# Kernel optimization log

Hardware: AMD Instinct MI355X
Metric: run time of the kernel (lower is better)

The kernel has to match this reference:

```python
import jax, jax.numpy as jnp
import numpy as np
import math

N_NODES = 50000
N_EDGES = 800000
D_IN = 128
HID = 128  # layer dims: 128 -> 128 -> 64 -> 32


def _glorot(key, fan_in, fan_out):
    lim = math.sqrt(6.0 / (fan_in + fan_out))
    return jax.random.uniform(key, (fan_in, fan_out), jnp.float32, -lim, lim)


def setup_inputs() -> dict:
    key = jax.random.key(0)
    ks = jax.random.split(key, 9)
    x = jax.random.normal(ks[0], (N_NODES, D_IN), dtype=jnp.float32)
    edge_index = jax.random.randint(ks[1], (2, N_EDGES), 0, N_NODES, dtype=jnp.int64)
    edge_attr = jax.random.uniform(ks[2], (N_EDGES,), dtype=jnp.float32)
    return {
        "x": x,
        "edge_index": edge_index,
        "edge_attr": edge_attr,
        "W1": _glorot(ks[3], D_IN, HID),      "b1": jnp.zeros((HID,), jnp.float32),
        "W2": _glorot(ks[4], HID, HID // 2),  "b2": jnp.zeros((HID // 2,), jnp.float32),
        "W3": _glorot(ks[5], HID // 2, HID // 4), "b3": jnp.zeros((HID // 4,), jnp.float32),
    }


def _gcn_conv(h, W, b, src, dst, norm, n_nodes):
    # GCNConv: linear transform, then normalized scatter-add aggregation, then bias
    h = h @ W                                   # [N, F_out]
    msg = h[src] * norm[:, None]                # gather + scale, [E', F_out]
    out = jax.ops.segment_sum(msg, dst, num_segments=n_nodes)  # scatter-add
    return out + b


def reference(x, edge_index, edge_attr, W1, b1, W2, b2, W3, b3):
    n = x.shape[0]
    # add self-loops with weight 1.0 (PyG GCNConv default)
    loop = jnp.arange(n, dtype=edge_index.dtype)
    src = jnp.concatenate([edge_index[0], loop])
    dst = jnp.concatenate([edge_index[1], loop])
    w = jnp.concatenate([edge_attr, jnp.ones((n,), edge_attr.dtype)])
    # symmetric normalization: D^{-1/2} A_hat D^{-1/2}
    deg = jax.ops.segment_sum(w, dst, num_segments=n)
    dinv = jnp.where(deg > 0, jax.lax.rsqrt(jnp.maximum(deg, 1e-30)), 0.0)
    norm = dinv[src] * w * dinv[dst]            # [E + N]

    h = jax.nn.relu(_gcn_conv(x, W1, b1, src, dst, norm, n))
    # dropout is identity in eval mode
    h = jax.nn.relu(_gcn_conv(h, W2, b2, src, dst, norm, n))
    h = _gcn_conv(h, W3, b3, src, dst, norm, n)
    return h
```

## Files before the change

### kernel.cpp

```cpp
#include <hip/hip_runtime.h>
#include <hip/hip_bf16.h>

#define BLK 256
#define SCAT_NB 512
#define BIN_SHIFT 8

typedef unsigned short ushort_t;
typedef unsigned int uint_t;
typedef unsigned long long ull_t;
typedef __attribute__((ext_vector_type(8))) short bf16x8;
typedef __attribute__((ext_vector_type(4))) float f32x4;

static __device__ __forceinline__ float bf2f(ushort_t u) {
    return __uint_as_float((uint_t)u << 16);
}
static __device__ __forceinline__ ushort_t f2bf(float f) {
    __hip_bfloat16 h = __float2bfloat16(f);
    return *reinterpret_cast<ushort_t*>(&h);
}


__global__ __launch_bounds__(256) void k_pre(const int* __restrict__ eidx,
                                             int* __restrict__ bcnt,
                                             int nbins, int epb, int E,
                                             const float* __restrict__ x,
                                             ushort_t* __restrict__ xb, int n4,
                                             const float* __restrict__ W1, ushort_t* __restrict__ Wt1,
                                             const float* __restrict__ W2, ushort_t* __restrict__ Wt2,
                                             const float* __restrict__ W3, ushort_t* __restrict__ Wt3) {
    const int b = blockIdx.x;
    const int t = threadIdx.x;
    if (b < SCAT_NB) {
        __shared__ int h[256];
        h[t] = 0;
        __syncthreads();
        const int base = b * epb;
        const int lim  = min(base + epb, E);
        for (int e = base + t; e < lim; e += 256)
            atomicAdd(&h[eidx[E + e] >> BIN_SHIFT], 1);
        __syncthreads();
        if (t < nbins) bcnt[(size_t)t * SCAT_NB + b] = h[t];
    } else {
        int i = (b - SCAT_NB) * 256 + t;
        if (i < n4) {
            float4 v = ((const float4*)x)[i];
            ((ushort4*)xb)[i] = make_ushort4(f2bf(v.x), f2bf(v.y), f2bf(v.z), f2bf(v.w));
        } else {
            int j = i - n4;
            if (j < 128 * 128) {
                int r = j / 128, c = j % 128;
                Wt1[(size_t)c * 128 + r] = f2bf(W1[j]);
            } else if (j < 128 * 128 + 128 * 64) {
                j -= 128 * 128;
                int r = j / 64, c = j % 64;
                Wt2[(size_t)c * 128 + r] = f2bf(W2[j]);
            } else if (j < 128 * 128 + 128 * 64 + 64 * 32) {
                j -= 128 * 128 + 128 * 64;
                int r = j / 32, c = j % 32;
                Wt3[(size_t)c * 64 + r] = f2bf(W3[j]);
            }
        }
    }
}


__global__ __launch_bounds__(256) void k_scan1(const int* __restrict__ cnt,
                                               int* rowptr, int* bsum, int n) {
    __shared__ int tile[256];
    const int t = threadIdx.x;
    const int i = blockIdx.x * 256 + t;
    int v = (i < n) ? cnt[i] : 0;
    tile[t] = v;
    __syncthreads();
    for (int off = 1; off < 256; off <<= 1) {
        int x = (t >= off) ? tile[t - off] : 0;
        __syncthreads();
        tile[t] += x;
        __syncthreads();
    }
    if (i < n) rowptr[i] = tile[t] - v;
    if (t == 255) bsum[blockIdx.x] = tile[255];
}

__global__ __launch_bounds__(256) void k_scan2x(int* a, int n) {
    __shared__ int tile[256];
    __shared__ int carry_s;
    const int t = threadIdx.x;
    if (t == 0) carry_s = 0;
    __syncthreads();
    for (int base = 0; base < n; base += 256) {
        int i = base + t;
        int v = (i < n) ? a[i] : 0;
        tile[t] = v;
        __syncthreads();
        for (int off = 1; off < 256; off <<= 1) {
            int x = (t >= off) ? tile[t - off] : 0;
            __syncthreads();
            tile[t] += x;
            __syncthreads();
        }
        int carry = carry_s;
        if (i < n) a[i] = carry + tile[t] - v;
        __syncthreads();
        if (t == 255) carry_s = carry + tile[255];
        __syncthreads();
    }
}



__global__ __launch_bounds__(256) void k_bin_scatter(const int* __restrict__ eidx,
                                                     const float* __restrict__ ea,
                                                     const int* __restrict__ ebofs,
                                                     const int* __restrict__ bsumB,
                                                     int2* __restrict__ binned_sd,
                                                     float* __restrict__ binned_ea,
                                                     int nbins, int epb, int E) {
    __shared__ int h[256];
    __shared__ int lofs[256];
    const int t = threadIdx.x;
    h[t] = 0;
    if (t < nbins) {
        int idx = t * SCAT_NB + blockIdx.x;
        lofs[t] = ebofs[idx] + bsumB[idx >> 8];
    }
    __syncthreads();
    const int base = blockIdx.x * epb;
    const int lim  = min(base + epb, E);
    for (int e = base + t; e < lim; e += 256) {
        int s = eidx[e];
        int d = eidx[E + e];
        float w = ea[e];
        int bin = d >> BIN_SHIFT;
        int r = atomicAdd(&h[bin], 1);
        int pos = lofs[bin] + r;
        binned_sd[pos] = make_int2(s, d);
        binned_ea[pos] = w;
    }
}

__global__ __launch_bounds__(256) void k_bin_hist(const int2* __restrict__ binned_sd,
                                                  const float* __restrict__ binned_ea,
                                                  const int* __restrict__ ebofs,
                                                  const int* __restrict__ bsumB,
                                                  float* __restrict__ dinv,
                                                  float* __restrict__ selfn,
                                                  int* __restrict__ rowptr,
                                                  int nbins, int N, int E) {
    __shared__ ull_t hs[256];
    __shared__ int sc[256];
    const int t = threadIdx.x;
    const int b = blockIdx.x;
    hs[t] = 0ull;
    __syncthreads();
    const int i0 = b * SCAT_NB;
    const int start = ebofs[i0] + bsumB[i0 >> 8];
    int end = E;
    if (b + 1 < nbins) {
        int i1 = (b + 1) * SCAT_NB;
        end = ebofs[i1] + bsumB[i1 >> 8];
    }
    for (int i = start + t; i < end; i += 256) {
        int d = binned_sd[i].y;
        float w = binned_ea[i];
        atomicAdd(&hs[d & 255], (1ull << 40) | (ull_t)(w * 4294967296.0f));
    }
    __syncthreads();
    int v = (int)(hs[t] >> 40);
    sc[t] = v;
    __syncthreads();
    for (int off = 1; off < 256; off <<= 1) {
        int x = (t >= off) ? sc[t - off] : 0;
        __syncthreads();
        sc[t] += x;
        __syncthreads();
    }
    const int node = (b << BIN_SHIFT) + t;
    if (node < N) {
        ull_t s = hs[t];
        float dg = 1.0f + (float)(s & ((1ull << 40) - 1)) * (1.0f / 4294967296.0f);
        dinv[node]  = rsqrtf(dg);
        selfn[node] = 1.0f / dg;
        rowptr[node] = start + sc[t] - v;
    }
    if (b == 0 && t == 0) rowptr[N] = E;
}

__global__ __launch_bounds__(256) void k_bin_emit(const int2* __restrict__ binned_sd,
                                                  const float* __restrict__ binned_ea,
                                                  const int* __restrict__ ebofs,
                                                  const int* __restrict__ bsumB,
                                                  const int* __restrict__ rowptr,
                                                  const float* __restrict__ dinv,
                                                  int* __restrict__ csr_src,
                                                  float* __restrict__ csr_val,
                                                  int nbins, int E) {
    __shared__ int c2[256];
    const int t = threadIdx.x;
    const int b = blockIdx.x;
    c2[t] = 0;
    __syncthreads();
    const int i0 = b * SCAT_NB;
    const int start = ebofs[i0] + bsumB[i0 >> 8];
    int end = E;
    if (b + 1 < nbins) {
        int i1 = (b + 1) * SCAT_NB;
        end = ebofs[i1] + bsumB[i1 >> 8];
    }
    for (int i = start + t; i < end; i += 256) {
        int2 sd = binned_sd[i];
        float w = binned_ea[i];
        int r = atomicAdd(&c2[sd.y & 255], 1);
        int pos = rowptr[sd.y] + r;
        csr_src[pos] = sd.x;
        csr_val[pos] = dinv[sd.x] * w * dinv[sd.y];
    }
}


template <int FIN, int FOUT>
__global__ __launch_bounds__(256) void k_gemm_mfma(const ushort_t* __restrict__ A,
                                                   const ushort_t* __restrict__ Wt,
                                                   ushort_t* __restrict__ C, int n) {
    constexpr int NT = FOUT / 16;
    constexpr int NK = FIN / 32;
    const int wave = threadIdx.x >> 6;
    const int lane = threadIdx.x & 63;
    const int r0 = (blockIdx.x * 4 + wave) * 32;
    if (r0 >= n) return;

    const int l15 = lane & 15;
    const int kg  = lane >> 4;
    const int arow0 = min(r0 + l15, n - 1);
    const int arow1 = min(r0 + 16 + l15, n - 1);

    f32x4 acc0[NT], acc1[NT];
#pragma unroll
    for (int c = 0; c < NT; ++c) { acc0[c] = (f32x4)(0.0f); acc1[c] = (f32x4)(0.0f); }

    const ushort_t* Ap0 = A + (size_t)arow0 * FIN + kg * 8;
    const ushort_t* Ap1 = A + (size_t)arow1 * FIN + kg * 8;
    const ushort_t* Bp  = Wt + (size_t)l15 * FIN + kg * 8;

#pragma unroll 1
    for (int ks = 0; ks < NK; ++ks) {
        bf16x8 a0 = *(const bf16x8*)(Ap0 + ks * 32);
        bf16x8 a1 = *(const bf16x8*)(Ap1 + ks * 32);
#pragma unroll
        for (int c = 0; c < NT; ++c) {
            bf16x8 bfr = *(const bf16x8*)(Bp + (size_t)c * 16 * FIN + ks * 32);
            acc0[c] = __builtin_amdgcn_mfma_f32_16x16x32_bf16(a0, bfr, acc0[c], 0, 0, 0);
            acc1[c] = __builtin_amdgcn_mfma_f32_16x16x32_bf16(a1, bfr, acc1[c], 0, 0, 0);
        }
    }

#pragma unroll
    for (int g = 0; g < 2; ++g) {
        const int rbase = r0 + g * 16 + kg * 4;
#pragma unroll
        for (int c = 0; c < NT; ++c) {
#pragma unroll
            for (int j = 0; j < 4; ++j) {
                int row = rbase + j;
                float val = (g == 0) ? acc0[c][j] : acc1[c][j];
                if (row < n) C[(size_t)row * FOUT + c * 16 + l15] = f2bf(val);
            }
        }
    }
}


template <int FOUT, bool RELU, bool OBF16>
__global__ __launch_bounds__(256) void k_agg(const ushort_t* __restrict__ H,
                                             const float* __restrict__ selfn,
                                             const int* __restrict__ rowptr,
                                             const int* __restrict__ csr_src,
                                             const float* __restrict__ csr_val,
                                             const float* __restrict__ bias,
                                             void* __restrict__ outv, int n) {
    constexpr int LPN = FOUT / 4;
    constexpr int NPW = 64 / LPN;
    const int wave = threadIdx.x >> 6;
    const int lane = threadIdx.x & 63;
    const int sub  = lane / LPN;
    const int f4   = lane % LPN;
    const int node = (blockIdx.x * 4 + wave) * NPW + sub;
    if (node >= n) return;

    const ushort_t* __restrict__ Hf = H + 4 * f4;

    const float sn = selfn[node];
    ushort4 hv = *(const ushort4*)(Hf + (size_t)node * FOUT);
    float a0 = sn * bf2f(hv.x);
    float a1 = sn * bf2f(hv.y);
    float a2 = sn * bf2f(hv.z);
    float a3 = sn * bf2f(hv.w);

    const int e0 = rowptr[node], e1 = rowptr[node + 1];
    int e = e0;
    for (; e + 8 <= e1; e += 8) {
        int   s0 = csr_src[e+0], s1 = csr_src[e+1], s2 = csr_src[e+2], s3 = csr_src[e+3];
        int   s4 = csr_src[e+4], s5 = csr_src[e+5], s6 = csr_src[e+6], s7 = csr_src[e+7];
        float v0 = csr_val[e+0], v1 = csr_val[e+1], v2 = csr_val[e+2], v3 = csr_val[e+3];
        float v4 = csr_val[e+4], v5 = csr_val[e+5], v6 = csr_val[e+6], v7 = csr_val[e+7];
        ushort4 m0 = *(const ushort4*)(Hf + (size_t)s0 * FOUT);
        ushort4 m1 = *(const ushort4*)(Hf + (size_t)s1 * FOUT);
        ushort4 m2 = *(const ushort4*)(Hf + (size_t)s2 * FOUT);
        ushort4 m3 = *(const ushort4*)(Hf + (size_t)s3 * FOUT);
        ushort4 m4 = *(const ushort4*)(Hf + (size_t)s4 * FOUT);
        ushort4 m5 = *(const ushort4*)(Hf + (size_t)s5 * FOUT);
        ushort4 m6 = *(const ushort4*)(Hf + (size_t)s6 * FOUT);
        ushort4 m7 = *(const ushort4*)(Hf + (size_t)s7 * FOUT);
        a0 += v0 * bf2f(m0.x); a1 += v0 * bf2f(m0.y); a2 += v0 * bf2f(m0.z); a3 += v0 * bf2f(m0.w);
        a0 += v1 * bf2f(m1.x); a1 += v1 * bf2f(m1.y); a2 += v1 * bf2f(m1.z); a3 += v1 * bf2f(m1.w);
        a0 += v2 * bf2f(m2.x); a1 += v2 * bf2f(m2.y); a2 += v2 * bf2f(m2.z); a3 += v2 * bf2f(m2.w);
        a0 += v3 * bf2f(m3.x); a1 += v3 * bf2f(m3.y); a2 += v3 * bf2f(m3.z); a3 += v3 * bf2f(m3.w);
        a0 += v4 * bf2f(m4.x); a1 += v4 * bf2f(m4.y); a2 += v4 * bf2f(m4.z); a3 += v4 * bf2f(m4.w);
        a0 += v5 * bf2f(m5.x); a1 += v5 * bf2f(m5.y); a2 += v5 * bf2f(m5.z); a3 += v5 * bf2f(m5.w);
        a0 += v6 * bf2f(m6.x); a1 += v6 * bf2f(m6.y); a2 += v6 * bf2f(m6.z); a3 += v6 * bf2f(m6.w);
        a0 += v7 * bf2f(m7.x); a1 += v7 * bf2f(m7.y); a2 += v7 * bf2f(m7.z); a3 += v7 * bf2f(m7.w);
    }
    for (; e + 2 <= e1; e += 2) {
        int   s0 = csr_src[e+0], s1 = csr_src[e+1];
        float v0 = csr_val[e+0], v1 = csr_val[e+1];
        ushort4 m0 = *(const ushort4*)(Hf + (size_t)s0 * FOUT);
        ushort4 m1 = *(const ushort4*)(Hf + (size_t)s1 * FOUT);
        a0 += v0 * bf2f(m0.x); a1 += v0 * bf2f(m0.y); a2 += v0 * bf2f(m0.z); a3 += v0 * bf2f(m0.w);
        a0 += v1 * bf2f(m1.x); a1 += v1 * bf2f(m1.y); a2 += v1 * bf2f(m1.z); a3 += v1 * bf2f(m1.w);
    }
    if (e < e1) {
        int   s0 = csr_src[e];
        float v0 = csr_val[e];
        ushort4 m0 = *(const ushort4*)(Hf + (size_t)s0 * FOUT);
        a0 += v0 * bf2f(m0.x); a1 += v0 * bf2f(m0.y); a2 += v0 * bf2f(m0.z); a3 += v0 * bf2f(m0.w);
    }

    float4 bv = *(const float4*)(bias + 4 * f4);
    a0 += bv.x; a1 += bv.y; a2 += bv.z; a3 += bv.w;
    if (RELU) {
        a0 = fmaxf(a0, 0.f); a1 = fmaxf(a1, 0.f);
        a2 = fmaxf(a2, 0.f); a3 = fmaxf(a3, 0.f);
    }
    if (OBF16) {
        ushort4 o = make_ushort4(f2bf(a0), f2bf(a1), f2bf(a2), f2bf(a3));
        *(ushort4*)((ushort_t*)outv + (size_t)node * FOUT + 4 * f4) = o;
    } else {
        *(float4*)((float*)outv + (size_t)node * FOUT + 4 * f4) = make_float4(a0, a1, a2, a3);
    }
}


extern "C" void kernel_launch(void* const* d_in, const int* in_sizes, int n_in,
                              void* d_out, int out_size, void* d_ws, size_t ws_size,
                              hipStream_t stream) {
    const float* x    = (const float*)d_in[0];
    const int*   eidx = (const int*)d_in[1];
    const float* ea   = (const float*)d_in[2];
    const float* W1   = (const float*)d_in[3];
    const float* b1   = (const float*)d_in[4];
    const float* W2   = (const float*)d_in[5];
    const float* b2   = (const float*)d_in[6];
    const float* W3   = (const float*)d_in[7];
    const float* b3   = (const float*)d_in[8];

    const int N = in_sizes[0] / 128;
    const int E = in_sizes[2];

    const int nbins = (N + 255) >> BIN_SHIFT;
    const int epb   = (E + SCAT_NB - 1) / SCAT_NB;
    const int nbc   = nbins * SCAT_NB;
    const int gBC   = (nbc + BLK - 1) / BLK;

    char*  base = (char*)d_ws;
    size_t off  = 0;
    auto carve = [&](size_t nbytes) -> void* {
        void* p = base + off;
        off = (off + nbytes + 255) & ~(size_t)255;
        return p;
    };
    int*   bcnt      = (int*)  carve((size_t)nbc * 4);
    int*   ebofs     = (int*)  carve((size_t)nbc * 4);
    int*   bsumB     = (int*)  carve((size_t)512 * 4);
    int2*  binned_sd = (int2*) carve((size_t)E * 8);
    float* binned_ea = (float*)carve((size_t)E * 4);
    float* dinv      = (float*)carve((size_t)N * 4);
    float* selfn     = (float*)carve((size_t)N * 4);
    int*   rowptr    = (int*)  carve((size_t)(N + 1) * 4);
    int*   csr_src   = (int*)  carve((size_t)E * 4);
    float* csr_val   = (float*)carve((size_t)E * 4);
    ushort_t* bufA   = (ushort_t*)carve((size_t)N * 128 * 2);
    ushort_t* bufB   = (ushort_t*)carve((size_t)N * 128 * 2);
    ushort_t* Wt1    = (ushort_t*)carve((size_t)128 * 128 * 2);
    ushort_t* Wt2    = (ushort_t*)carve((size_t)64 * 128 * 2);
    ushort_t* Wt3    = (ushort_t*)carve((size_t)32 * 64 * 2);
    (void)ws_size;

    const int n4 = N * 128 / 4;
    const int gPre = SCAT_NB + (n4 + 128 * 128 + 128 * 64 + 64 * 32 + 255) / 256;
    const int gR = (N + 127) / 128;

    k_pre<<<gPre, BLK, 0, stream>>>(eidx, bcnt, nbins, epb, E,
                                    x, bufB, n4, W1, Wt1, W2, Wt2, W3, Wt3);
    k_scan1<<<gBC, BLK, 0, stream>>>(bcnt, ebofs, bsumB, nbc);
    k_scan2x<<<1, BLK, 0, stream>>>(bsumB, gBC);
    k_bin_scatter<<<SCAT_NB, BLK, 0, stream>>>(eidx, ea, ebofs, bsumB, binned_sd, binned_ea, nbins, epb, E);
    k_bin_hist<<<nbins, BLK, 0, stream>>>(binned_sd, binned_ea, ebofs, bsumB, dinv, selfn, rowptr, nbins, N, E);
    k_bin_emit<<<nbins, BLK, 0, stream>>>(binned_sd, binned_ea, ebofs, bsumB, rowptr, dinv,
                                          csr_src, csr_val, nbins, E);

    k_gemm_mfma<128, 128><<<gR, BLK, 0, stream>>>(bufB, Wt1, bufA, N);
    k_agg<128, true, true><<<(N + 7) / 8, BLK, 0, stream>>>(bufA, selfn, rowptr, csr_src, csr_val, b1, bufB, N);

    k_gemm_mfma<128, 64><<<gR, BLK, 0, stream>>>(bufB, Wt2, bufA, N);
    k_agg<64, true, true><<<(N + 15) / 16, BLK, 0, stream>>>(bufA, selfn, rowptr, csr_src, csr_val, b2, bufB, N);

    k_gemm_mfma<64, 32><<<gR, BLK, 0, stream>>>(bufB, Wt3, bufA, N);
    k_agg<32, false, false><<<(N + 31) / 32, BLK, 0, stream>>>(bufA, selfn, rowptr, csr_src, csr_val, b3, d_out, N);
}
```

Measured before the change: 151.5 us.

## Fuse CSR build kernels, pack binned edges, fold dinv into GEMM, read fp32 x

Merges the degree-histogram and CSR-emit kernels into one kernel that stages each bin's edges in LDS. Binned edges are packed into a single uint2 holding (src<<8 | dst&255, weight). The source-side dinv scaling moves into the GEMM epilogue, so CSR values only carry the destination dinv and the separate selfn array is dropped. The first GEMM converts fp32 x to bf16 on the fly, which removes the bf16 copy of x. Together these remove a kernel launch, extra passes over the edge list and the x conversion traffic, at the cost of heavy LDS use (about 52 KB per block) and a fallback path for large bins.

After: 142.1 us (median of 2 runs). 1.07x faster.

```diff
diff --git a/kernel.cpp b/kernel.cpp
--- a/kernel.cpp
+++ b/kernel.cpp
@@ -4,6 +4,7 @@
 #define BLK 256
 #define SCAT_NB 512
 #define BIN_SHIFT 8
+#define STAGE_CAP 6144
 
 typedef unsigned short ushort_t;
 typedef unsigned int uint_t;
@@ -20,11 +21,10 @@
 }
 
 
+
 __global__ __launch_bounds__(256) void k_pre(const int* __restrict__ eidx,
                                              int* __restrict__ bcnt,
                                              int nbins, int epb, int E,
-                                             const float* __restrict__ x,
-                                             ushort_t* __restrict__ xb, int n4,
                                              const float* __restrict__ W1, ushort_t* __restrict__ Wt1,
                                              const float* __restrict__ W2, ushort_t* __restrict__ Wt2,
                                              const float* __restrict__ W3, ushort_t* __restrict__ Wt3) {
@@ -41,24 +41,18 @@
         __syncthreads();
         if (t < nbins) bcnt[(size_t)t * SCAT_NB + b] = h[t];
     } else {
-        int i = (b - SCAT_NB) * 256 + t;
-        if (i < n4) {
-            float4 v = ((const float4*)x)[i];
-            ((ushort4*)xb)[i] = make_ushort4(f2bf(v.x), f2bf(v.y), f2bf(v.z), f2bf(v.w));
-        } else {
-            int j = i - n4;
-            if (j < 128 * 128) {
-                int r = j / 128, c = j % 128;
-                Wt1[(size_t)c * 128 + r] = f2bf(W1[j]);
-            } else if (j < 128 * 128 + 128 * 64) {
-                j -= 128 * 128;
-                int r = j / 64, c = j % 64;
-                Wt2[(size_t)c * 128 + r] = f2bf(W2[j]);
-            } else if (j < 128 * 128 + 128 * 64 + 64 * 32) {
-                j -= 128 * 128 + 128 * 64;
-                int r = j / 32, c = j % 32;
-                Wt3[(size_t)c * 64 + r] = f2bf(W3[j]);
-            }
+        int j = (b - SCAT_NB) * 256 + t;
+        if (j < 128 * 128) {
+            int r = j / 128, c = j % 128;
+            Wt1[(size_t)c * 128 + r] = f2bf(W1[j]);
+        } else if (j < 128 * 128 + 128 * 64) {
+            j -= 128 * 128;
+            int r = j / 64, c = j % 64;
+            Wt2[(size_t)c * 128 + r] = f2bf(W2[j]);
+        } else if (j < 128 * 128 + 128 * 64 + 64 * 32) {
+            j -= 128 * 128 + 128 * 64;
+            int r = j / 32, c = j % 32;
+            Wt3[(size_t)c * 64 + r] = f2bf(W3[j]);
         }
     }
 }
@@ -113,8 +107,7 @@
                                                      const float* __restrict__ ea,
                                                      const int* __restrict__ ebofs,
                                                      const int* __restrict__ bsumB,
-                                                     int2* __restrict__ binned_sd,
-                                                     float* __restrict__ binned_ea,
+                                                     uint2* __restrict__ binned,
                                                      int nbins, int epb, int E) {
     __shared__ int h[256];
     __shared__ int lofs[256];
@@ -134,24 +127,29 @@
         int bin = d >> BIN_SHIFT;
         int r = atomicAdd(&h[bin], 1);
         int pos = lofs[bin] + r;
-        binned_sd[pos] = make_int2(s, d);
-        binned_ea[pos] = w;
-    }
-}
-
-__global__ __launch_bounds__(256) void k_bin_hist(const int2* __restrict__ binned_sd,
-                                                  const float* __restrict__ binned_ea,
-                                                  const int* __restrict__ ebofs,
-                                                  const int* __restrict__ bsumB,
-                                                  float* __restrict__ dinv,
-                                                  float* __restrict__ selfn,
-                                                  int* __restrict__ rowptr,
-                                                  int nbins, int N, int E) {
+        binned[pos] = make_uint2(((uint_t)s << 8) | (uint_t)(d & 255), __float_as_uint(w));
+    }
+}
+
+
+__global__ __launch_bounds__(256) void k_bin_finish(const uint2* __restrict__ binned,
+                                                    const int* __restrict__ ebofs,
+                                                    const int* __restrict__ bsumB,
+                                                    float* __restrict__ dinv,
+                                                    int* __restrict__ rowptr,
+                                                    int* __restrict__ csr_src,
+                                                    float* __restrict__ csr_val,
+                                                    int nbins, int N, int E) {
+    __shared__ uint2 stage[STAGE_CAP];
     __shared__ ull_t hs[256];
-    __shared__ int sc[256];
+    __shared__ int   sc[256];
+    __shared__ int   rp[256];
+    __shared__ float dl[256];
+    __shared__ int   c2[256];
     const int t = threadIdx.x;
     const int b = blockIdx.x;
     hs[t] = 0ull;
+    c2[t] = 0;
     __syncthreads();
     const int i0 = b * SCAT_NB;
     const int start = ebofs[i0] + bsumB[i0 >> 8];
@@ -160,12 +158,25 @@
         int i1 = (b + 1) * SCAT_NB;
         end = ebofs[i1] + bsumB[i1 >> 8];
     }
-    for (int i = start + t; i < end; i += 256) {
-        int d = binned_sd[i].y;
-        float w = binned_ea[i];
-        atomicAdd(&hs[d & 255], (1ull << 40) | (ull_t)(w * 4294967296.0f));
-    }
-    __syncthreads();
+    const int cnt = end - start;
+    const bool fits = (cnt <= STAGE_CAP);
+
+    if (fits) {
+        for (int i = t; i < cnt; i += 256) {
+            uint2 p = binned[start + i];
+            stage[i] = p;
+            atomicAdd(&hs[p.x & 255],
+                      (1ull << 40) | (ull_t)(__uint_as_float(p.y) * 4294967296.0f));
+        }
+    } else {
+        for (int i = start + t; i < end; i += 256) {
+            uint2 p = binned[i];
+            atomicAdd(&hs[p.x & 255],
+                      (1ull << 40) | (ull_t)(__uint_as_float(p.y) * 4294967296.0f));
+        }
+    }
+    __syncthreads();
+
     int v = (int)(hs[t] >> 40);
     sc[t] = v;
     __syncthreads();
@@ -175,52 +186,47 @@
         sc[t] += x;
         __syncthreads();
     }
-    const int node = (b << BIN_SHIFT) + t;
-    if (node < N) {
+    {
         ull_t s = hs[t];
         float dg = 1.0f + (float)(s & ((1ull << 40) - 1)) * (1.0f / 4294967296.0f);
-        dinv[node]  = rsqrtf(dg);
-        selfn[node] = 1.0f / dg;
-        rowptr[node] = start + sc[t] - v;
-    }
-    if (b == 0 && t == 0) rowptr[N] = E;
-}
-
-__global__ __launch_bounds__(256) void k_bin_emit(const int2* __restrict__ binned_sd,
-                                                  const float* __restrict__ binned_ea,
-                                                  const int* __restrict__ ebofs,
-                                                  const int* __restrict__ bsumB,
-                                                  const int* __restrict__ rowptr,
-                                                  const float* __restrict__ dinv,
-                                                  int* __restrict__ csr_src,
-                                                  float* __restrict__ csr_val,
-                                                  int nbins, int E) {
-    __shared__ int c2[256];
-    const int t = threadIdx.x;
-    const int b = blockIdx.x;
-    c2[t] = 0;
-    __syncthreads();
-    const int i0 = b * SCAT_NB;
-    const int start = ebofs[i0] + bsumB[i0 >> 8];
-    int end = E;
-    if (b + 1 < nbins) {
-        int i1 = (b + 1) * SCAT_NB;
-        end = ebofs[i1] + bsumB[i1 >> 8];
-    }
-    for (int i = start + t; i < end; i += 256) {
-        int2 sd = binned_sd[i];
-        float w = binned_ea[i];
-        int r = atomicAdd(&c2[sd.y & 255], 1);
-        int pos = rowptr[sd.y] + r;
-        csr_src[pos] = sd.x;
-        csr_val[pos] = dinv[sd.x] * w * dinv[sd.y];
-    }
-}
-
-
-template <int FIN, int FOUT>
-__global__ __launch_bounds__(256) void k_gemm_mfma(const ushort_t* __restrict__ A,
+        float di = rsqrtf(dg);
+        dl[t] = di;
+        rp[t] = start + sc[t] - v;
+        const int node = (b << BIN_SHIFT) + t;
+        if (node < N) {
+            dinv[node]   = di;
+            rowptr[node] = rp[t];
+        }
+        if (b == 0 && t == 0) rowptr[N] = E;
+    }
+    __syncthreads();
+
+    if (fits) {
+        for (int i = t; i < cnt; i += 256) {
+            uint2 p = stage[i];
+            int d8 = p.x & 255;
+            int r = atomicAdd(&c2[d8], 1);
+            int pos = rp[d8] + r;
+            csr_src[pos] = (int)(p.x >> 8);
+            csr_val[pos] = __uint_as_float(p.y) * dl[d8];
+        }
+    } else {
+        for (int i = start + t; i < end; i += 256) {
+            uint2 p = binned[i];
+            int d8 = p.x & 255;
+            int r = atomicAdd(&c2[d8], 1);
+            int pos = rp[d8] + r;
+            csr_src[pos] = (int)(p.x >> 8);
+            csr_val[pos] = __uint_as_float(p.y) * dl[d8];
+        }
+    }
+}
+
+
+template <int FIN, int FOUT, bool AF32>
+__global__ __launch_bounds__(256) void k_gemm_mfma(const void* __restrict__ Av,
                                                    const ushort_t* __restrict__ Wt,
+                                                   const float* __restrict__ dinv,
                                                    ushort_t* __restrict__ C, int n) {
     constexpr int NT = FOUT / 16;
     constexpr int NK = FIN / 32;
@@ -238,14 +244,30 @@
 #pragma unroll
     for (int c = 0; c < NT; ++c) { acc0[c] = (f32x4)(0.0f); acc1[c] = (f32x4)(0.0f); }
 
-    const ushort_t* Ap0 = A + (size_t)arow0 * FIN + kg * 8;
-    const ushort_t* Ap1 = A + (size_t)arow1 * FIN + kg * 8;
-    const ushort_t* Bp  = Wt + (size_t)l15 * FIN + kg * 8;
+    const ushort_t* Bp = Wt + (size_t)l15 * FIN + kg * 8;
 
 #pragma unroll 1
     for (int ks = 0; ks < NK; ++ks) {
-        bf16x8 a0 = *(const bf16x8*)(Ap0 + ks * 32);
-        bf16x8 a1 = *(const bf16x8*)(Ap1 + ks * 32);
+        bf16x8 a0, a1;
+        if (AF32) {
+            const float* A = (const float*)Av;
+            const float* p0 = A + (size_t)arow0 * FIN + kg * 8 + ks * 32;
+            const float* p1 = A + (size_t)arow1 * FIN + kg * 8 + ks * 32;
+            float4 u0 = *(const float4*)p0, u1 = *(const float4*)(p0 + 4);
+            float4 w0 = *(const float4*)p1, w1 = *(const float4*)(p1 + 4);
+            a0[0] = (short)f2bf(u0.x); a0[1] = (short)f2bf(u0.y);
+            a0[2] = (short)f2bf(u0.z); a0[3] = (short)f2bf(u0.w);
+            a0[4] = (short)f2bf(u1.x); a0[5] = (short)f2bf(u1.y);
+            a0[6] = (short)f2bf(u1.z); a0[7] = (short)f2bf(u1.w);
+            a1[0] = (short)f2bf(w0.x); a1[1] = (short)f2bf(w0.y);
+            a1[2] = (short)f2bf(w0.z); a1[3] = (short)f2bf(w0.w);
+            a1[4] = (short)f2bf(w1.x); a1[5] = (short)f2bf(w1.y);
+            a1[6] = (short)f2bf(w1.z); a1[7] = (short)f2bf(w1.w);
+        } else {
+            const ushort_t* A = (const ushort_t*)Av;
+            a0 = *(const bf16x8*)(A + (size_t)arow0 * FIN + kg * 8 + ks * 32);
+            a1 = *(const bf16x8*)(A + (size_t)arow1 * FIN + kg * 8 + ks * 32);
+        }
 #pragma unroll
         for (int c = 0; c < NT; ++c) {
             bf16x8 bfr = *(const bf16x8*)(Bp + (size_t)c * 16 * FIN + ks * 32);
@@ -258,12 +280,15 @@
     for (int g = 0; g < 2; ++g) {
         const int rbase = r0 + g * 16 + kg * 4;
 #pragma unroll
-        for (int c = 0; c < NT; ++c) {
+        for (int j = 0; j < 4; ++j) {
+            int row = rbase + j;
+            if (row < n) {
+                float dscale = dinv[row];
 #pragma unroll
-            for (int j = 0; j < 4; ++j) {
-                int row = rbase + j;
-                float val = (g == 0) ? acc0[c][j] : acc1[c][j];
-                if (row < n) C[(size_t)row * FOUT + c * 16 + l15] = f2bf(val);
+                for (int c = 0; c < NT; ++c) {
+                    float val = (g == 0) ? acc0[c][j] : acc1[c][j];
+                    C[(size_t)row * FOUT + c * 16 + l15] = f2bf(val * dscale);
+                }
             }
         }
     }
@@ -272,7 +297,7 @@
 
 template <int FOUT, bool RELU, bool OBF16>
 __global__ __launch_bounds__(256) void k_agg(const ushort_t* __restrict__ H,
-                                             const float* __restrict__ selfn,
+                                             const float* __restrict__ dinv,
                                              const int* __restrict__ rowptr,
                                              const int* __restrict__ csr_src,
                                              const float* __restrict__ csr_val,
@@ -289,7 +314,7 @@
 
     const ushort_t* __restrict__ Hf = H + 4 * f4;
 
-    const float sn = selfn[node];
+    const float sn = dinv[node];
     ushort4 hv = *(const ushort4*)(Hf + (size_t)node * FOUT);
     float a0 = sn * bf2f(hv.x);
     float a1 = sn * bf2f(hv.y);
@@ -381,10 +406,8 @@
     int*   bcnt      = (int*)  carve((size_t)nbc * 4);
     int*   ebofs     = (int*)  carve((size_t)nbc * 4);
     int*   bsumB     = (int*)  carve((size_t)512 * 4);
-    int2*  binned_sd = (int2*) carve((size_t)E * 8);
-    float* binned_ea = (float*)carve((size_t)E * 4);
+    uint2* binned    = (uint2*)carve((size_t)E * 8);
     float* dinv      = (float*)carve((size_t)N * 4);
-    float* selfn     = (float*)carve((size_t)N * 4);
     int*   rowptr    = (int*)  carve((size_t)(N + 1) * 4);
     int*   csr_src   = (int*)  carve((size_t)E * 4);
     float* csr_val   = (float*)carve((size_t)E * 4);
@@ -395,25 +418,23 @@
     ushort_t* Wt3    = (ushort_t*)carve((size_t)32 * 64 * 2);
     (void)ws_size;
 
-    const int n4 = N * 128 / 4;
-    const int gPre = SCAT_NB + (n4 + 128 * 128 + 128 * 64 + 64 * 32 + 255) / 256;
+    const int wtot = 128 * 128 + 128 * 64 + 64 * 32;
+    const int gPre = SCAT_NB + (wtot + 255) / 256;
     const int gR = (N + 127) / 128;
 
-    k_pre<<<gPre, BLK, 0, stream>>>(eidx, bcnt, nbins, epb, E,
-                                    x, bufB, n4, W1, Wt1, W2, Wt2, W3, Wt3);
+    k_pre<<<gPre, BLK, 0, stream>>>(eidx, bcnt, nbins, epb, E, W1, Wt1, W2, Wt2, W3, Wt3);
     k_scan1<<<gBC, BLK, 0, stream>>>(bcnt, ebofs, bsumB, nbc);
     k_scan2x<<<1, BLK, 0, stream>>>(bsumB, gBC);
-    k_bin_scatter<<<SCAT_NB, BLK, 0, stream>>>(eidx, ea, ebofs, bsumB, binned_sd, binned_ea, nbins, epb, E);
-    k_bin_hist<<<nbins, BLK, 0, stream>>>(binned_sd, binned_ea, ebofs, bsumB, dinv, selfn, rowptr, nbins, N, E);
-    k_bin_emit<<<nbins, BLK, 0, stream>>>(binned_sd, binned_ea, ebofs, bsumB, rowptr, dinv,
-                                          csr_src, csr_val, nbins, E);
-
-    k_gemm_mfma<128, 128><<<gR, BLK, 0, stream>>>(bufB, Wt1, bufA, N);
-    k_agg<128, true, true><<<(N + 7) / 8, BLK, 0, stream>>>(bufA, selfn, rowptr, csr_src, csr_val, b1, bufB, N);
-
-    k_gemm_mfma<128, 64><<<gR, BLK, 0, stream>>>(bufB, Wt2, bufA, N);
-    k_agg<64, true, true><<<(N + 15) / 16, BLK, 0, stream>>>(bufA, selfn, rowptr, csr_src, csr_val, b2, bufB, N);
-
-    k_gemm_mfma<64, 32><<<gR, BLK, 0, stream>>>(bufB, Wt3, bufA, N);
-    k_agg<32, false, false><<<(N + 31) / 32, BLK, 0, stream>>>(bufA, selfn, rowptr, csr_src, csr_val, b3, d_out, N);
-}
+    k_bin_scatter<<<SCAT_NB, BLK, 0, stream>>>(eidx, ea, ebofs, bsumB, binned, nbins, epb, E);
+    k_bin_finish<<<nbins, BLK, 0, stream>>>(binned, ebofs, bsumB, dinv, rowptr,
+                                            csr_src, csr_val, nbins, N, E);
+
+    k_gemm_mfma<128, 128, true><<<gR, BLK, 0, stream>>>(x, Wt1, dinv, bufA, N);
+    k_agg<128, true, true><<<(N + 7) / 8, BLK, 0, stream>>>(bufA, dinv, rowptr, csr_src, csr_val, b1, bufB, N);
+
+    k_gemm_mfma<128, 64, false><<<gR, BLK, 0, stream>>>(bufB, Wt2, dinv, bufA, N);
+    k_agg<64, true, true><<<(N + 15) / 16, BLK, 0, stream>>>(bufA, dinv, rowptr, csr_src, csr_val, b2, bufB, N);
+
+    k_gemm_mfma<64, 32, false><<<gR, BLK, 0, stream>>>(bufB, Wt3, dinv, bufA, N);
+    k_agg<32, false, false><<<(N + 31) / 32, BLK, 0, stream>>>(bufA, dinv, rowptr, csr_src, csr_val, b3, d_out, N);
+}
```
